# Performance work log

Hardware: AMD Instinct MI355X
Metric: run time of the kernel (lower is better)

Reference implementation:

```python
import jax, jax.numpy as jnp
import numpy as np

B, IDIM, ODIM, MSIZE = 8192, 4096, 4096, 128
ICOUNT = (IDIM + MSIZE - 1) // MSIZE        # 32
MCOUNT = (max(IDIM, ODIM) + MSIZE - 1) // MSIZE  # 32
OCOUNT = (ODIM + MSIZE - 1) // MSIZE        # 32


def setup_inputs() -> dict:
    key = jax.random.key(0)
    ks = jax.random.split(key, 7)
    s_in = 1.0 / np.sqrt(ICOUNT)
    s_m = 1.0 / np.sqrt(MSIZE)
    s_out = 1.0 / np.sqrt(MCOUNT)
    return {
        "x": jax.random.normal(ks[0], (B, IDIM), dtype=jnp.float32),
        "W_in": jax.random.normal(ks[1], (MCOUNT, ICOUNT), dtype=jnp.float32) * s_in,
        "b_in": jax.random.normal(ks[2], (MCOUNT,), dtype=jnp.float32) * s_in,
        "W_mods": jax.random.normal(ks[3], (MCOUNT, MSIZE, MSIZE), dtype=jnp.float32) * s_m,
        "b_mods": jax.random.normal(ks[4], (MCOUNT, MSIZE), dtype=jnp.float32) * s_m,
        "W_out": jax.random.normal(ks[5], (OCOUNT, MCOUNT), dtype=jnp.float32) * s_out,
        "b_out": jax.random.normal(ks[6], (OCOUNT,), dtype=jnp.float32) * s_out,
        "odim": ODIM,
    }


def reference(x, W_in, b_in, W_mods, b_mods, W_out, b_out, odim):
    msize = W_mods.shape[-1]
    b = x.shape[0]
    idim = x.shape[-1]
    rem = idim % msize  # static
    if rem != 0:
        x = jnp.pad(x, ((0, 0), (0, msize - rem)))
    icount = x.shape[-1] // msize
    # reshape to blocks then tail_permute (swap last two axes)
    x = x.reshape(b, icount, msize).swapaxes(-1, -2)      # [B, msize, icount]
    x = jnp.einsum('bmi,ci->bmc', x, W_in) + b_in          # fcin -> [B, msize, mcount]
    x = x.swapaxes(-1, -2)                                 # [B, mcount, msize]
    # per-block submodule: Linear(msize->msize) per block, vectorized over blocks
    x = jnp.einsum('bcm,cnm->bcn', x, W_mods) + b_mods     # [B, mcount, msize]
    x = x.swapaxes(-1, -2)                                 # [B, msize, mcount]
    x = jnp.einsum('bmc,oc->bmo', x, W_out) + b_out        # fcout -> [B, msize, ocount]
    x = x.reshape(b, -1)[:, :odim]                         # [B, odim]
    return x  # act = Identity
```

## Files before the change

kernel.cpp:

```cpp
#include <hip/hip_runtime.h>
#include <hip/hip_bf16.h>
#include <stdint.h>


#define BT    16
#define NTHR  512
#define GRID  512
#define IDIM  4096
#define ODIM  4096

typedef __attribute__((ext_vector_type(8))) __bf16 bf16x8;
typedef __attribute__((ext_vector_type(4))) float  floatx4;

union BF8 { uint32_t w[4]; unsigned short h[8]; bf16x8 v; };

__device__ __forceinline__ unsigned short f2bf(float f) {
    uint32_t u = __builtin_bit_cast(uint32_t, f);
    u += 0x7fffu + ((u >> 16) & 1u);
    return (unsigned short)(u >> 16);
}

#define YP_BT 132
#define YP_C  2116
#define WP_BT 36
#define WP_N  584
#define SCR_ELEMS (16 * WP_N)

template<bool WBF16>
__global__ __launch_bounds__(NTHR, 1)
void tinymod_fused(const float* __restrict__ x,
                   const float* __restrict__ W_in,
                   const float* __restrict__ b_in,
                   const void*  __restrict__ wmods,
                   const float* __restrict__ b_mods,
                   const float* __restrict__ W_out,
                   const float* __restrict__ b_out,
                   float* __restrict__ out)
{
    __shared__ unsigned short ylds[32 * YP_C] __attribute__((aligned(16)));
    __shared__ unsigned short scr[SCR_ELEMS]  __attribute__((aligned(16)));

    const int tid  = threadIdx.x;
    const int lane = tid & 63;
    const int wave = tid >> 6;
    const int l15  = lane & 15;
    const int grp  = lane >> 4;
    const int row0 = blockIdx.x * BT;

    const float bin0 = b_in[l15],  bin1 = b_in[16 + l15];
    const float bo0  = b_out[l15], bo1  = b_out[16 + l15];
    BF8 winf[2], woutf[2];
    #pragma unroll
    for (int cc = 0; cc < 2; cc++) {
        const float* p = W_in  + (l15 + 16*cc) * 32 + grp * 8;
        const float* q = W_out + (l15 + 16*cc) * 32 + grp * 8;
        #pragma unroll
        for (int j = 0; j < 8; j++) { winf[cc].h[j] = f2bf(p[j]); woutf[cc].h[j] = f2bf(q[j]); }
    }

    const int smp = tid & 15;
    const int sbt = (tid >> 4) & 15;
    const int sih = tid >> 8;
    const float* xb = x + (row0 + sbt) * IDIM + smp;

    float xr[16];
    #pragma unroll
    for (int p = 0; p < 2; p++) {
        const int i0 = (sih + 2*p) * 8;
        #pragma unroll
        for (int j = 0; j < 8; j++) xr[p*8 + j] = xb[(i0 + j) * 128];
    }

    for (int mb = 0; mb < 8; mb++) {
        #pragma unroll
        for (int p = 0; p < 2; p++) {
            const int i0 = (sih + 2*p) * 8;
            BF8 t;
            #pragma unroll
            for (int j = 0; j < 8; j++) t.h[j] = f2bf(xr[p*8 + j]);
            uint4 val; val.x = t.w[0]; val.y = t.w[1]; val.z = t.w[2]; val.w = t.w[3];
            *(uint4*)&scr[(smp*16 + sbt)*32 + i0] = val;
        }
        __syncthreads();

        float xr2[16];
        if (mb < 7) {
            #pragma unroll
            for (int p = 0; p < 2; p++) {
                const int i0 = (sih + 2*p) * 8;
                #pragma unroll
                for (int j = 0; j < 8; j++) xr2[p*8 + j] = xb[(i0 + j) * 128 + (mb + 1) * 16];
            }
        }

        unsigned short yh[2][2][4];
        #pragma unroll
        for (int mm = 0; mm < 2; mm++) {
            const int mp = 2*wave + mm;
            BF8 a;
            const uint4 av = *(const uint4*)&scr[(mp*16 + l15)*32 + grp*8];
            a.w[0] = av.x; a.w[1] = av.y; a.w[2] = av.z; a.w[3] = av.w;
            #pragma unroll
            for (int cc = 0; cc < 2; cc++) {
                floatx4 acc = {0.f, 0.f, 0.f, 0.f};
                acc = __builtin_amdgcn_mfma_f32_16x16x32_bf16(a.v, winf[cc].v, acc, 0, 0, 0);
                const float bi = cc ? bin1 : bin0;
                #pragma unroll
                for (int r = 0; r < 4; r++) yh[mm][cc][r] = f2bf(acc[r] + bi);
            }
        }
        #pragma unroll
        for (int cc = 0; cc < 2; cc++)
            #pragma unroll
            for (int r = 0; r < 4; r++) {
                const int c  = l15 + 16*cc;
                const int bt = grp*4 + r;
                const uint32_t pk = (uint32_t)yh[0][cc][r] | ((uint32_t)yh[1][cc][r] << 16);
                *(uint32_t*)&ylds[c*YP_C + bt*YP_BT + mb*16 + 2*wave] = pk;
            }
        __syncthreads();
        if (mb < 7) {
            #pragma unroll
            for (int q = 0; q < 16; q++) xr[q] = xr2[q];
        }
    }

    const unsigned short* __restrict__ wm16 = (const unsigned short*)wmods;
    const float*          __restrict__ wm32 = (const float*)wmods;

    for (int nb = 0; nb < 8; nb++) {
        floatx4 acc[4];
        float   bm[4];
        #pragma unroll
        for (int ci = 0; ci < 4; ci++) {
            const int c = 4*wave + ci;
            bm[ci] = b_mods[c*128 + nb*16 + l15];
            const int ybase = c*YP_C + l15*YP_BT + grp*8;
            const int wbase = (c*128 + nb*16 + l15)*128 + grp*8;
            floatx4 s = {0.f, 0.f, 0.f, 0.f};
            #pragma unroll
            for (int kc = 0; kc < 4; kc++) {
                BF8 a;
                const uint2 u0 = *(const uint2*)&ylds[ybase + kc*32];
                const uint2 u1 = *(const uint2*)&ylds[ybase + kc*32 + 4];
                a.w[0] = u0.x; a.w[1] = u0.y; a.w[2] = u1.x; a.w[3] = u1.y;
                BF8 b;
                if (WBF16) {
                    const uint4 bv = *(const uint4*)&wm16[wbase + kc*32];
                    b.w[0] = bv.x; b.w[1] = bv.y; b.w[2] = bv.z; b.w[3] = bv.w;
                } else {
                    const float* wp = wm32 + wbase + kc*32;
                    #pragma unroll
                    for (int j = 0; j < 8; j++) b.h[j] = f2bf(wp[j]);
                }
                s = __builtin_amdgcn_mfma_f32_16x16x32_bf16(a.v, b.v, s, 0, 0, 0);
            }
            acc[ci] = s;
        }
        #pragma unroll
        for (int r = 0; r < 4; r++) {
            unsigned short h[4];
            #pragma unroll
            for (int ci = 0; ci < 4; ci++) h[ci] = f2bf(acc[ci][r] + bm[ci]);
            uint2 pk;
            pk.x = (uint32_t)h[0] | ((uint32_t)h[1] << 16);
            pk.y = (uint32_t)h[2] | ((uint32_t)h[3] << 16);
            *(uint2*)&scr[l15*WP_N + (grp*4 + r)*WP_BT + 4*wave] = pk;
        }
        __syncthreads();

        #pragma unroll
        for (int mm = 0; mm < 2; mm++) {
            const int mp = 2*wave + mm;
            BF8 a;
            const int off = mp*WP_N + l15*WP_BT + grp*8;
            const uint2 u0 = *(const uint2*)&scr[off];
            const uint2 u1 = *(const uint2*)&scr[off + 4];
            a.w[0] = u0.x; a.w[1] = u0.y; a.w[2] = u1.x; a.w[3] = u1.y;
            #pragma unroll
            for (int oc = 0; oc < 2; oc++) {
                floatx4 v = {0.f, 0.f, 0.f, 0.f};
                v = __builtin_amdgcn_mfma_f32_16x16x32_bf16(a.v, woutf[oc].v, v, 0, 0, 0);
                const float bo = oc ? bo1 : bo0;
                float* po = out + row0*ODIM + (nb*16 + mp)*32 + l15 + 16*oc;
                #pragma unroll
                for (int r = 0; r < 4; r++) {
                    const int bt = grp*4 + r;
                    po[bt*ODIM] = v[r] + bo;
                }
            }
        }
        __syncthreads();
    }
}

__global__ void wmods_to_bf16(const float* __restrict__ w, unsigned short* __restrict__ o) {
    const int i = (blockIdx.x * 256 + threadIdx.x) * 4;
    const float4 f = *(const float4*)(w + i);
    uint2 pk;
    pk.x = (uint32_t)f2bf(f.x) | ((uint32_t)f2bf(f.y) << 16);
    pk.y = (uint32_t)f2bf(f.z) | ((uint32_t)f2bf(f.w) << 16);
    *(uint2*)(o + i) = pk;
}

extern "C" void kernel_launch(void* const* d_in, const int* in_sizes, int n_in,
                              void* d_out, int out_size, void* d_ws, size_t ws_size,
                              hipStream_t stream)
{
    const float* x     = (const float*)d_in[0];
    const float* W_in  = (const float*)d_in[1];
    const float* b_in  = (const float*)d_in[2];
    const float* Wm    = (const float*)d_in[3];
    const float* b_m   = (const float*)d_in[4];
    const float* W_out = (const float*)d_in[5];
    const float* b_out = (const float*)d_in[6];
    float* out = (float*)d_out;

    const size_t wm_elems = 32u * 128u * 128u;
    if (ws_size >= wm_elems * sizeof(unsigned short)) {
        unsigned short* wbf = (unsigned short*)d_ws;
        wmods_to_bf16<<<(int)(wm_elems / (256 * 4)), 256, 0, stream>>>(Wm, wbf);
        tinymod_fused<true><<<GRID, NTHR, 0, stream>>>(x, W_in, b_in, (const void*)wbf,
                                                       b_m, W_out, b_out, out);
    } else {
        tinymod_fused<false><<<GRID, NTHR, 0, stream>>>(x, W_in, b_in, (const void*)Wm,
                                                        b_m, W_out, b_out, out);
    }
}
```

Before: 311.9 us.

## Halve rows per block, swizzle LDS layout, and raise occupancy to four blocks

Each block now handles 8 batch rows instead of 16, which doubles the grid and shrinks LDS use so launch bounds can allow four blocks per CU. The first stage has each wave compute its own row straight from registers, with no staging through scratch LDS and no per-step barriers. Stage outputs go into an XOR-swizzled LDS layout to cut bank conflicts. With only 8 rows, half of each 16-row MFMA tile is wasted, so W_mods is streamed twice as often per output row.

```diff
diff --git a/kernel.cpp b/kernel.cpp
--- a/kernel.cpp
+++ b/kernel.cpp
@@ -1,11 +1,10 @@
 #include <hip/hip_runtime.h>
-#include <hip/hip_bf16.h>
 #include <stdint.h>
 
 
-#define BT    16
+#define BT    8
 #define NTHR  512
-#define GRID  512
+#define GRID  1024
 #define IDIM  4096
 #define ODIM  4096
 
@@ -20,14 +19,14 @@
     return (unsigned short)(u >> 16);
 }
 
-#define YP_BT 132
-#define YP_C  2116
-#define WP_BT 36
-#define WP_N  584
-#define SCR_ELEMS (16 * WP_N)
+#define YROW 132
+__device__ __forceinline__ int yaddr(int c, int bt, int m) {
+    return (c * 8 + bt) * YROW + ((((m >> 2) ^ (c & 7))) << 2) + (m & 3);
+}
+#define WROW 36
 
 template<bool WBF16>
-__global__ __launch_bounds__(NTHR, 1)
+__global__ __launch_bounds__(NTHR, 4)
 void tinymod_fused(const float* __restrict__ x,
                    const float* __restrict__ W_in,
                    const float* __restrict__ b_in,
@@ -37,8 +36,8 @@
                    const float* __restrict__ b_out,
                    float* __restrict__ out)
 {
-    __shared__ unsigned short ylds[32 * YP_C] __attribute__((aligned(16)));
-    __shared__ unsigned short scr[SCR_ELEMS]  __attribute__((aligned(16)));
+    __shared__ unsigned short ylds[256 * YROW]    __attribute__((aligned(16)));
+    __shared__ unsigned short wch [16 * 8 * WROW] __attribute__((aligned(16)));
 
     const int tid  = threadIdx.x;
     const int lane = tid & 63;
@@ -58,75 +57,43 @@
         for (int j = 0; j < 8; j++) { winf[cc].h[j] = f2bf(p[j]); woutf[cc].h[j] = f2bf(q[j]); }
     }
 
-    const int smp = tid & 15;
-    const int sbt = (tid >> 4) & 15;
-    const int sih = tid >> 8;
-    const float* xb = x + (row0 + sbt) * IDIM + smp;
-
-    float xr[16];
+    const float* xb = x + (row0 + wave) * IDIM + l15;
+    float xr[8];
     #pragma unroll
-    for (int p = 0; p < 2; p++) {
-        const int i0 = (sih + 2*p) * 8;
-        #pragma unroll
-        for (int j = 0; j < 8; j++) xr[p*8 + j] = xb[(i0 + j) * 128];
-    }
+    for (int j = 0; j < 8; j++) xr[j] = xb[(grp*8 + j) * 128];
 
     for (int mb = 0; mb < 8; mb++) {
-        #pragma unroll
-        for (int p = 0; p < 2; p++) {
-            const int i0 = (sih + 2*p) * 8;
-            BF8 t;
-            #pragma unroll
-            for (int j = 0; j < 8; j++) t.h[j] = f2bf(xr[p*8 + j]);
-            uint4 val; val.x = t.w[0]; val.y = t.w[1]; val.z = t.w[2]; val.w = t.w[3];
-            *(uint4*)&scr[(smp*16 + sbt)*32 + i0] = val;
-        }
-        __syncthreads();
-
-        float xr2[16];
+        float xn[8];
         if (mb < 7) {
             #pragma unroll
-            for (int p = 0; p < 2; p++) {
-                const int i0 = (sih + 2*p) * 8;
-                #pragma unroll
-                for (int j = 0; j < 8; j++) xr2[p*8 + j] = xb[(i0 + j) * 128 + (mb + 1) * 16];
-            }
-        }
-
-        unsigned short yh[2][2][4];
-        #pragma unroll
-        for (int mm = 0; mm < 2; mm++) {
-            const int mp = 2*wave + mm;
-            BF8 a;
-            const uint4 av = *(const uint4*)&scr[(mp*16 + l15)*32 + grp*8];
-            a.w[0] = av.x; a.w[1] = av.y; a.w[2] = av.z; a.w[3] = av.w;
-            #pragma unroll
-            for (int cc = 0; cc < 2; cc++) {
-                floatx4 acc = {0.f, 0.f, 0.f, 0.f};
-                acc = __builtin_amdgcn_mfma_f32_16x16x32_bf16(a.v, winf[cc].v, acc, 0, 0, 0);
-                const float bi = cc ? bin1 : bin0;
-                #pragma unroll
-                for (int r = 0; r < 4; r++) yh[mm][cc][r] = f2bf(acc[r] + bi);
-            }
-        }
-        #pragma unroll
-        for (int cc = 0; cc < 2; cc++)
-            #pragma unroll
-            for (int r = 0; r < 4; r++) {
-                const int c  = l15 + 16*cc;
-                const int bt = grp*4 + r;
-                const uint32_t pk = (uint32_t)yh[0][cc][r] | ((uint32_t)yh[1][cc][r] << 16);
-                *(uint32_t*)&ylds[c*YP_C + bt*YP_BT + mb*16 + 2*wave] = pk;
-            }
-        __syncthreads();
+            for (int j = 0; j < 8; j++) xn[j] = xb[(grp*8 + j) * 128 + (mb + 1) * 16];
+        }
+        BF8 a;
+        #pragma unroll
+        for (int j = 0; j < 8; j++) a.h[j] = f2bf(xr[j]);
+        #pragma unroll
+        for (int cc = 0; cc < 2; cc++) {
+            floatx4 acc = {0.f, 0.f, 0.f, 0.f};
+            acc = __builtin_amdgcn_mfma_f32_16x16x32_bf16(a.v, winf[cc].v, acc, 0, 0, 0);
+            const float bi = cc ? bin1 : bin0;
+            unsigned short h[4];
+            #pragma unroll
+            for (int r = 0; r < 4; r++) h[r] = f2bf(acc[r] + bi);
+            uint2 pk;
+            pk.x = (uint32_t)h[0] | ((uint32_t)h[1] << 16);
+            pk.y = (uint32_t)h[2] | ((uint32_t)h[3] << 16);
+            *(uint2*)&ylds[yaddr(l15 + 16*cc, wave, mb*16 + grp*4)] = pk;
+        }
         if (mb < 7) {
             #pragma unroll
-            for (int q = 0; q < 16; q++) xr[q] = xr2[q];
-        }
-    }
+            for (int j = 0; j < 8; j++) xr[j] = xn[j];
+        }
+    }
+    __syncthreads();
 
     const unsigned short* __restrict__ wm16 = (const unsigned short*)wmods;
     const float*          __restrict__ wm32 = (const float*)wmods;
+    const int btA = l15 & 7;
 
     for (int nb = 0; nb < 8; nb++) {
         floatx4 acc[4];
@@ -135,62 +102,66 @@
         for (int ci = 0; ci < 4; ci++) {
             const int c = 4*wave + ci;
             bm[ci] = b_mods[c*128 + nb*16 + l15];
-            const int ybase = c*YP_C + l15*YP_BT + grp*8;
-            const int wbase = (c*128 + nb*16 + l15)*128 + grp*8;
             floatx4 s = {0.f, 0.f, 0.f, 0.f};
             #pragma unroll
             for (int kc = 0; kc < 4; kc++) {
-                BF8 a;
-                const uint2 u0 = *(const uint2*)&ylds[ybase + kc*32];
-                const uint2 u1 = *(const uint2*)&ylds[ybase + kc*32 + 4];
-                a.w[0] = u0.x; a.w[1] = u0.y; a.w[2] = u1.x; a.w[3] = u1.y;
+                const int m0 = kc*32 + grp*8;
+                BF8 a2;
+                const uint2 u0 = *(const uint2*)&ylds[yaddr(c, btA, m0)];
+                const uint2 u1 = *(const uint2*)&ylds[yaddr(c, btA, m0 + 4)];
+                a2.w[0] = u0.x; a2.w[1] = u0.y; a2.w[2] = u1.x; a2.w[3] = u1.y;
                 BF8 b;
+                const int wbase = (c*128 + nb*16 + l15)*128 + kc*32 + grp*8;
                 if (WBF16) {
-                    const uint4 bv = *(const uint4*)&wm16[wbase + kc*32];
+                    const uint4 bv = *(const uint4*)&wm16[wbase];
                     b.w[0] = bv.x; b.w[1] = bv.y; b.w[2] = bv.z; b.w[3] = bv.w;
                 } else {
-                    const float* wp = wm32 + wbase + kc*32;
+                    const float* wp = wm32 + wbase;
                     #pragma unroll
                     for (int j = 0; j < 8; j++) b.h[j] = f2bf(wp[j]);
                 }
-                s = __builtin_amdgcn_mfma_f32_16x16x32_bf16(a.v, b.v, s, 0, 0, 0);
+                s = __builtin_amdgcn_mfma_f32_16x16x32_bf16(a2.v, b.v, s, 0, 0, 0);
             }
             acc[ci] = s;
         }
-        #pragma unroll
-        for (int r = 0; r < 4; r++) {
-            unsigned short h[4];
-            #pragma unroll
-            for (int ci = 0; ci < 4; ci++) h[ci] = f2bf(acc[ci][r] + bm[ci]);
-            uint2 pk;
-            pk.x = (uint32_t)h[0] | ((uint32_t)h[1] << 16);
-            pk.y = (uint32_t)h[2] | ((uint32_t)h[3] << 16);
-            *(uint2*)&scr[l15*WP_N + (grp*4 + r)*WP_BT + 4*wave] = pk;
+        if (grp < 2) {
+            #pragma unroll
+            for (int r = 0; r < 4; r++) {
+                const int bt = grp*4 + r;
+                unsigned short h[4];
+                #pragma unroll
+                for (int ci = 0; ci < 4; ci++) h[ci] = f2bf(acc[ci][r] + bm[ci]);
+                uint2 pk;
+                pk.x = (uint32_t)h[0] | ((uint32_t)h[1] << 16);
+                pk.y = (uint32_t)h[2] | ((uint32_t)h[3] << 16);
+                *(uint2*)&wch[(l15*8 + bt)*WROW + 4*wave] = pk;
+            }
         }
         __syncthreads();
 
-        #pragma unroll
-        for (int mm = 0; mm < 2; mm++) {
-            const int mp = 2*wave + mm;
-            BF8 a;
-            const int off = mp*WP_N + l15*WP_BT + grp*8;
-            const uint2 u0 = *(const uint2*)&scr[off];
-            const uint2 u1 = *(const uint2*)&scr[off + 4];
-            a.w[0] = u0.x; a.w[1] = u0.y; a.w[2] = u1.x; a.w[3] = u1.y;
-            #pragma unroll
-            for (int oc = 0; oc < 2; oc++) {
-                floatx4 v = {0.f, 0.f, 0.f, 0.f};
-                v = __builtin_amdgcn_mfma_f32_16x16x32_bf16(a.v, woutf[oc].v, v, 0, 0, 0);
-                const float bo = oc ? bo1 : bo0;
-                float* po = out + row0*ODIM + (nb*16 + mp)*32 + l15 + 16*oc;
-                #pragma unroll
-                for (int r = 0; r < 4; r++) {
-                    const int bt = grp*4 + r;
-                    po[bt*ODIM] = v[r] + bo;
-                }
+        const int np = 2*wave + (l15 >> 3);
+        BF8 a3;
+        {
+            const int off = (np*8 + btA)*WROW + grp*8;
+            const uint2 u0 = *(const uint2*)&wch[off];
+            const uint2 u1 = *(const uint2*)&wch[off + 4];
+            a3.w[0] = u0.x; a3.w[1] = u0.y; a3.w[2] = u1.x; a3.w[3] = u1.y;
+        }
+        __syncthreads();
+
+        #pragma unroll
+        for (int oc = 0; oc < 2; oc++) {
+            floatx4 v = {0.f, 0.f, 0.f, 0.f};
+            v = __builtin_amdgcn_mfma_f32_16x16x32_bf16(a3.v, woutf[oc].v, v, 0, 0, 0);
+            const float bo = oc ? bo1 : bo0;
+            #pragma unroll
+            for (int r = 0; r < 4; r++) {
+                const int R   = grp*4 + r;
+                const int nlo = R >> 3;
+                const int bt  = R & 7;
+                out[(row0 + bt)*ODIM + (nb*16 + 2*wave + nlo)*32 + oc*16 + l15] = v[r] + bo;
             }
         }
-        __syncthreads();
     }
 }
 
```

After: 354.4 us. 13.6% more time.
